# Kernel tuning notes

Measured on AMD Instinct MI355X. Metric: run time of the kernel, lower is better.

The kernel has to match this reference:

```python
import jax, jax.numpy as jnp
import numpy as np

N = 50000   # nodes
E = 1600000 # edges
G = 512     # graphs in batch
IN_DIM, EMBED, H, D = 64, 128, 4, 32
D1, D2, D3 = 128, 64, 16
NEG_SLOPE = 0.2  # DGL GATConv default


def setup_inputs() -> dict:
    key = jax.random.key(0)
    ks = jax.random.split(key, 16)
    def glorot(k, shape):
        fan = shape[0] + shape[-1]
        return jax.random.normal(k, shape, jnp.float32) * jnp.sqrt(2.0 / fan)
    return {
        "feature": jax.random.normal(ks[0], (N, IN_DIM), jnp.float32),
        "src": jax.random.randint(ks[1], (E,), 0, N, jnp.int32),
        "dst": jax.random.randint(ks[2], (E,), 0, N, jnp.int32),
        "graph_ids": jnp.sort(jax.random.randint(ks[3], (N,), 0, G, jnp.int32)),
        "W0": glorot(ks[4], (IN_DIM, EMBED)), "b0": jnp.zeros((EMBED,), jnp.float32),
        "Wfc": glorot(ks[5], (EMBED, H * D)),
        "attn_l": glorot(ks[6], (H, D)), "attn_r": glorot(ks[7], (H, D)),
        "gat_bias": jnp.zeros((H * D,), jnp.float32),
        "W1": glorot(ks[8], (H * D, D1)), "b1": jnp.zeros((D1,), jnp.float32),
        "W2": glorot(ks[9], (D1, D2)), "b2": jnp.zeros((D2,), jnp.float32),
        "W3": glorot(ks[10], (D2, D3)), "b3": jnp.zeros((D3,), jnp.float32),
    }


def reference(feature, src, dst, graph_ids, W0, b0, Wfc, attn_l, attn_r,
              gat_bias, W1, b1, W2, b2, W3, b3):
    # initial dense embed
    h = feature @ W0 + b0                                   # [N, EMBED]
    # GATConv
    feat = (h @ Wfc).reshape(N, H, D)                       # [N,H,D]
    el = jnp.einsum('nhd,hd->nh', feat, attn_l)             # [N,H]
    er = jnp.einsum('nhd,hd->nh', feat, attn_r)
    e = jax.nn.leaky_relu(el[src] + er[dst], NEG_SLOPE)     # [E,H]
    # segment softmax over incoming edges of each dst node
    m = jax.ops.segment_max(e, dst, num_segments=N)         # [N,H]
    ex = jnp.exp(e - m[dst])                                # [E,H]
    denom = jax.ops.segment_sum(ex, dst, num_segments=N)    # [N,H]
    a = ex / denom[dst]                                     # [E,H]
    msg = a[:, :, None] * feat[src]                         # [E,H,D]
    rst = jax.ops.segment_sum(msg, dst, num_segments=N)     # [N,H,D]
    rst = rst + gat_bias.reshape(1, H, D)
    hn = rst.reshape(N, H * D)
    # AvgPooling per graph
    sums = jax.ops.segment_sum(hn, graph_ids, num_segments=G)           # [G,H*D]
    cnts = jax.ops.segment_sum(jnp.ones((N,), hn.dtype), graph_ids, num_segments=G)
    hg = sums / jnp.maximum(cnts, 1.0)[:, None]
    # dense head
    out = jax.nn.elu(hg)
    out = jax.nn.elu(out @ W1 + b1)
    out = jax.nn.elu(out @ W2 + b2)
    out = out @ W3 + b3                                     # [G, D3]
    atten = a[:, :, None]                                   # [E,H,1] like DGL
    return out, atten
```

## Files before the change

kernel.cpp:

```cpp
#include <hip/hip_runtime.h>
#include <hip/hip_fp16.h>
#include <math.h>

#define N_NODES 50000
#define E_EDGES 1600000
#define G_GRAPHS 512
#define IN_DIM 64
#define EMBED 128
#define HD 128
#define NHEAD 4
#define D1 128
#define D2 64
#define D3 16
#define NEG_SLOPE 0.2f
#define NB ((N_NODES + 127) >> 7)
#define PT_TILE 4096
#define PT_BLOCKS ((E_EDGES + PT_TILE - 1) / PT_TILE)
#define FB_CAP 8192
#define M2_EDGE_BLK ((E_EDGES + 511) / 512)

typedef float vfloat4 __attribute__((ext_vector_type(4)));
typedef float vfloat2 __attribute__((ext_vector_type(2)));
typedef unsigned short ushort_t;

static __device__ __forceinline__ float leaky(float x) { return x > 0.f ? x : NEG_SLOPE * x; }

__global__ void __launch_bounds__(256) k0hg(const int* __restrict__ dst, int* __restrict__ ghist,
                                            const float* __restrict__ W0, const float* __restrict__ b0,
                                            const float* __restrict__ Wfc, float* __restrict__ Wc,
                                            float* __restrict__ bc) {
    __shared__ int lh[NB];
    const int t = threadIdx.x;
    if (blockIdx.x < PT_BLOCKS) {
        for (int i = t; i < NB; i += 256) lh[i] = 0;
        __syncthreads();
        const long e0 = (long)blockIdx.x * PT_TILE;
#pragma unroll
        for (int k = 0; k < PT_TILE / 256; ++k) {
            long e = e0 + t + k * 256;
            if (e < E_EDGES) atomicAdd(&lh[dst[e] >> 7], 1);
        }
        __syncthreads();
        for (int i = t; i < NB; i += 256) {
            int v = lh[i];
            if (v) atomicAdd(&ghist[i], v);
        }
    } else {
        int tid = (int)(blockIdx.x - PT_BLOCKS) * 256 + t;
        if (tid < IN_DIM * HD) {
            int i = tid >> 7, j = tid & 127;
            float acc = 0.f;
            for (int k = 0; k < EMBED; ++k) acc += W0[i * EMBED + k] * Wfc[k * HD + j];
            Wc[tid] = acc;
        } else if (tid < IN_DIM * HD + HD) {
            int j = tid - IN_DIM * HD;
            float acc = 0.f;
            for (int k = 0; k < EMBED; ++k) acc += b0[k] * Wfc[k * HD + j];
            bc[j] = acc;
        }
    }
}

__global__ void __launch_bounds__(256) k1_gemm(const float* __restrict__ A,
                                               const float* __restrict__ W,
                                               const float* __restrict__ b,
                                               const float* __restrict__ attn_l,
                                               const float* __restrict__ attn_r,
                                               unsigned char* __restrict__ feat,
                                               float* __restrict__ el,
                                               float* __restrict__ er) {
    __shared__ __align__(16) float Ws[IN_DIM * HD];
    __shared__ __align__(16) float As[64][68];
    const int t = threadIdx.x;
    const int cc = t & 31, rt = t >> 5;
    const int c0 = cc * 4, r0 = rt * 8;
    const int row0 = blockIdx.x * 64;

    {
        const float4* Wg = (const float4*)W;
        float4* Wl = (float4*)Ws;
#pragma unroll
        for (int j = 0; j < (IN_DIM * HD / 4) / 256; ++j) Wl[t + j * 256] = Wg[t + j * 256];
    }
#pragma unroll
    for (int j = 0; j < 4; ++j) {
        int i2 = t + j * 256;
        int row = i2 >> 4, kq = i2 & 15;
        int gr = row0 + row;
        float4 v = (gr < N_NODES) ? *(const float4*)(A + (size_t)gr * IN_DIM + kq * 4)
                                  : make_float4(0.f, 0.f, 0.f, 0.f);
        *(float4*)&As[row][kq * 4] = v;
    }
    __syncthreads();

    float acc[8][4];
#pragma unroll
    for (int i = 0; i < 8; ++i)
#pragma unroll
        for (int j = 0; j < 4; ++j) acc[i][j] = 0.f;

    for (int k4 = 0; k4 < IN_DIM / 4; ++k4) {
        vfloat4 w0 = *(const vfloat4*)&Ws[(k4 * 4 + 0) * HD + c0];
        vfloat4 w1 = *(const vfloat4*)&Ws[(k4 * 4 + 1) * HD + c0];
        vfloat4 w2 = *(const vfloat4*)&Ws[(k4 * 4 + 2) * HD + c0];
        vfloat4 w3 = *(const vfloat4*)&Ws[(k4 * 4 + 3) * HD + c0];
#pragma unroll
        for (int i = 0; i < 8; ++i) {
            vfloat4 a = *(const vfloat4*)&As[r0 + i][k4 * 4];
#pragma unroll
            for (int j = 0; j < 4; ++j)
                acc[i][j] += a.x * w0[j] + a.y * w1[j] + a.z * w2[j] + a.w * w3[j];
        }
    }
    {
        vfloat4 bcv = *(const vfloat4*)(b + c0);
#pragma unroll
        for (int i = 0; i < 8; ++i)
#pragma unroll
            for (int j = 0; j < 4; ++j) acc[i][j] += bcv[j];
    }
#pragma unroll
    for (int i = 0; i < 8; ++i) {
        int gr = row0 + r0 + i;
        if (gr < N_NODES) {
            unsigned int ww = __builtin_amdgcn_cvt_pk_fp8_f32(acc[i][0], acc[i][1], 0, false);
            ww = __builtin_amdgcn_cvt_pk_fp8_f32(acc[i][2], acc[i][3], ww, true);
            *(unsigned int*)(feat + (size_t)gr * HD + c0) = ww;
        }
    }
    {
        vfloat4 al = *(const vfloat4*)(attn_l + c0);
        vfloat4 ar = *(const vfloat4*)(attn_r + c0);
        float pl[8], pr[8];
#pragma unroll
        for (int i = 0; i < 8; ++i) {
            pl[i] = acc[i][0] * al[0] + acc[i][1] * al[1] + acc[i][2] * al[2] + acc[i][3] * al[3];
            pr[i] = acc[i][0] * ar[0] + acc[i][1] * ar[1] + acc[i][2] * ar[2] + acc[i][3] * ar[3];
        }
#pragma unroll
        for (int off = 1; off <= 4; off <<= 1) {
#pragma unroll
            for (int i = 0; i < 8; ++i) {
                pl[i] += __shfl_xor(pl[i], off);
                pr[i] += __shfl_xor(pr[i], off);
            }
        }
        if ((cc & 7) == 0) {
            const int h = cc >> 3;
#pragma unroll
            for (int i = 0; i < 8; ++i) {
                int gr = row0 + r0 + i;
                if (gr < N_NODES) {
                    el[gr * 4 + h] = pl[i];
                    er[gr * 4 + h] = pr[i];
                }
            }
        }
    }
}

__global__ void __launch_bounds__(256) pt_partition(const int* __restrict__ src,
                                                    const int* __restrict__ dst,
                                                    const int* __restrict__ ghist,
                                                    int* __restrict__ cursor0,
                                                    unsigned int* __restrict__ part) {
    __shared__ int hist[4][NB];
    __shared__ int tot[NB], offs[NB], base_s[NB];
    __shared__ int lcur[4][NB];
    __shared__ int gt[NB], offsG[NB];
    __shared__ unsigned int stage[PT_TILE];
    const int t = threadIdx.x, lane = t & 63, wid = t >> 6;
    const long e0 = (long)blockIdx.x * PT_TILE;
    const int cnt = (int)min((long)PT_TILE, (long)E_EDGES - e0);
    for (int i = t; i < NB; i += 256) {
        hist[0][i] = 0; hist[1][i] = 0; hist[2][i] = 0; hist[3][i] = 0;
        gt[i] = ghist[i];
    }
    __syncthreads();
    unsigned int v[PT_TILE / 256];
#pragma unroll
    for (int k = 0; k < PT_TILE / 256; ++k) {
        int i = t + k * 256;
        if (i < cnt) {
            int d = dst[e0 + i];
            v[k] = ((unsigned int)d << 16) | (unsigned int)src[e0 + i];
            atomicAdd(&hist[wid][d >> 7], 1);
        } else v[k] = 0xFFFFFFFFu;
    }
    __syncthreads();
    for (int i = t; i < NB; i += 256) {
        int h0 = hist[0][i], h1 = hist[1][i], h2 = hist[2][i], h3 = hist[3][i];
        hist[0][i] = 0; hist[1][i] = h0; hist[2][i] = h0 + h1; hist[3][i] = h0 + h1 + h2;
        tot[i] = h0 + h1 + h2 + h3;
    }
    __syncthreads();
    if (wid == 0) {
        int run = 0;
        for (int c = 0; c < (NB + 63) / 64; ++c) {
            int i = c * 64 + lane;
            int vv = (i < NB) ? tot[i] : 0;
            int incl = vv;
#pragma unroll
            for (int off = 1; off < 64; off <<= 1) {
                int o = __shfl_up(incl, off, 64);
                if (lane >= off) incl += o;
            }
            if (i < NB) offs[i] = run + incl - vv;
            run += __shfl(incl, 63, 64);
        }
    } else if (wid == 1) {
        int run = 0;
        for (int c = 0; c < (NB + 63) / 64; ++c) {
            int i = c * 64 + lane;
            int vv = (i < NB) ? gt[i] : 0;
            int incl = vv;
#pragma unroll
            for (int off = 1; off < 64; off <<= 1) {
                int o = __shfl_up(incl, off, 64);
                if (lane >= off) incl += o;
            }
            if (i < NB) offsG[i] = run + incl - vv;
            run += __shfl(incl, 63, 64);
        }
    }
    __syncthreads();
    for (int i = t; i < NB; i += 256) {
        int tt = tot[i];
        base_s[i] = offsG[i] + (tt ? atomicAdd(&cursor0[i], tt) : 0);
        int ob = offs[i];
        lcur[0][i] = ob + hist[0][i];
        lcur[1][i] = ob + hist[1][i];
        lcur[2][i] = ob + hist[2][i];
        lcur[3][i] = ob + hist[3][i];
    }
    __syncthreads();
#pragma unroll
    for (int k = 0; k < PT_TILE / 256; ++k) {
        if (v[k] != 0xFFFFFFFFu) {
            int b = v[k] >> 23;
            int pos = atomicAdd(&lcur[wid][b], 1);
            stage[pos] = v[k];
        }
    }
    __syncthreads();
    for (int i = t; i < cnt; i += 256) {
        unsigned int p = stage[i];
        int b = p >> 23;
        part[base_s[b] + (i - offs[b])] = p & 0x7FFFFFu;
    }
}

__global__ void __launch_bounds__(256) fb_fill(const unsigned int* __restrict__ part,
                                               const int* __restrict__ ghist,
                                               int* __restrict__ rowstart,
                                               ushort_t* __restrict__ csr_src) {
    const int b = blockIdx.x, t = threadIdx.x, lane = t & 63, wid = t >> 6;
    __shared__ int degl[4][128], totl[128], offl[128], curl[4][128];
    __shared__ int red[4], s0s[2];
    __shared__ ushort_t lsrc[FB_CAP];
    {
        int partial = 0;
        for (int i = t; i < b; i += 256) partial += ghist[i];
#pragma unroll
        for (int off = 32; off; off >>= 1) partial += __shfl_xor(partial, off);
        if (lane == 0) red[wid] = partial;
        if (t < 128) { degl[0][t] = 0; degl[1][t] = 0; degl[2][t] = 0; degl[3][t] = 0; }
        __syncthreads();
        if (t == 0) {
            int s0 = red[0] + red[1] + red[2] + red[3];
            s0s[0] = s0;
            s0s[1] = s0 + ghist[b];
        }
        __syncthreads();
    }
    const int s0 = s0s[0], s1 = s0s[1];
    const int cnt = s1 - s0;
    for (int i = t; i < cnt; i += 256) {
        unsigned int p = part[s0 + i];
        atomicAdd(&degl[wid][p >> 16], 1);
    }
    __syncthreads();
    if (t < 128) {
        int d0 = degl[0][t], d1 = degl[1][t], d2 = degl[2][t], d3 = degl[3][t];
        degl[0][t] = 0; degl[1][t] = d0; degl[2][t] = d0 + d1; degl[3][t] = d0 + d1 + d2;
        totl[t] = d0 + d1 + d2 + d3;
    }
    __syncthreads();
    if (wid == 0) {
        int run = 0;
        for (int c = 0; c < 2; ++c) {
            int i = c * 64 + lane;
            int vv = totl[i];
            int incl = vv;
#pragma unroll
            for (int off = 1; off < 64; off <<= 1) {
                int o = __shfl_up(incl, off, 64);
                if (lane >= off) incl += o;
            }
            offl[i] = run + incl - vv;
            run += __shfl(incl, 63, 64);
        }
    }
    __syncthreads();
    if (t < 128) {
        int ob = offl[t];
        curl[0][t] = ob + degl[0][t];
        curl[1][t] = ob + degl[1][t];
        curl[2][t] = ob + degl[2][t];
        curl[3][t] = ob + degl[3][t];
        int node = (b << 7) + t;
        if (node < N_NODES) rowstart[node] = s0 + ob;
    }
    if (b == 0 && t == 0) rowstart[N_NODES] = E_EDGES;
    __syncthreads();
    if (cnt <= FB_CAP) {
        for (int i = t; i < cnt; i += 256) {
            unsigned int p = part[s0 + i];
            int pos = atomicAdd(&curl[wid][p >> 16], 1);
            lsrc[pos] = (ushort_t)(p & 0xFFFFu);
        }
        __syncthreads();
        for (int i = t; i < cnt; i += 256) csr_src[s0 + i] = lsrc[i];
    } else {
        for (int i = t; i < cnt; i += 256) {
            unsigned int p = part[s0 + i];
            int pos = atomicAdd(&curl[wid][p >> 16], 1);
            csr_src[s0 + pos] = (ushort_t)(p & 0xFFFFu);
        }
    }
}

__global__ void __launch_bounds__(256) k6_aggregate(
    const ushort_t* __restrict__ csr_src, const int* __restrict__ rowstart,
    const float* __restrict__ el, const float* __restrict__ er,
    const unsigned char* __restrict__ feat, const float* __restrict__ gat_bias,
    float* __restrict__ er_rd, float* __restrict__ hn) {
    __shared__ uint2 s_pk[4][64][4];
    const int wid = threadIdx.x >> 6;
    const int lane = threadIdx.x & 63;
    const int n = blockIdx.x * 4 + wid;
    if (n >= N_NODES) return;
    const int start = rowstart[n];
    const int end = rowstart[n + 1];
    const int deg = end - start;

    const int e0 = lane >> 2;
    const int h = lane & 3;
    const float erh = er[n * 4 + h];
    float sm = 0.f;
    for (int base = 0; base < deg; base += 16) {
        const int e = base + e0;
        if (e < deg) {
            const int s = csr_src[start + e];
            const float ex = __expf(leaky(el[s * 4 + h] + erh));
            sm += ex;
            if (e < 64)
                s_pk[wid][e][h] = make_uint2((unsigned int)s << 7, __float_as_uint(ex));
        }
    }
#pragma unroll
    for (int off = 4; off <= 32; off <<= 1) sm += __shfl_xor(sm, off);
    const float rd = sm > 0.f ? 1.f / sm : 0.f;
    if (lane < 4) {
        er_rd[(size_t)n * 8 + lane] = erh;
        er_rd[(size_t)n * 8 + 4 + lane] = rd;
    }

    const int g4 = lane >> 4, gl = lane & 15;
    const int h2 = gl >> 2;
    const float rdh = __shfl(rd, h2);
    vfloat2 acc0 = {0.f, 0.f}, acc1 = {0.f, 0.f}, acc2 = {0.f, 0.f}, acc3 = {0.f, 0.f};

    if (deg <= 64) {
        const uint2* pk = &s_pk[wid][0][h2];
        const unsigned char* fg = feat + (gl << 3);
        int idx = g4;
        for (; idx + 4 < deg; idx += 8) {
            const uint2 pA = pk[idx * 4];
            const uint2 pB = pk[(idx + 4) * 4];
            const uint2 wA = *(const uint2*)(fg + pA.x);
            const uint2 wB = *(const uint2*)(fg + pB.x);
            const float exA = __uint_as_float(pA.y);
            const float exB = __uint_as_float(pB.y);
            const vfloat2 eA = {exA, exA}, eB = {exB, exB};
            acc0 += eA * __builtin_amdgcn_cvt_pk_f32_fp8(wA.x, false);
            acc1 += eA * __builtin_amdgcn_cvt_pk_f32_fp8(wA.x, true);
            acc2 += eA * __builtin_amdgcn_cvt_pk_f32_fp8(wA.y, false);
            acc3 += eA * __builtin_amdgcn_cvt_pk_f32_fp8(wA.y, true);
            acc0 += eB * __builtin_amdgcn_cvt_pk_f32_fp8(wB.x, false);
            acc1 += eB * __builtin_amdgcn_cvt_pk_f32_fp8(wB.x, true);
            acc2 += eB * __builtin_amdgcn_cvt_pk_f32_fp8(wB.y, false);
            acc3 += eB * __builtin_amdgcn_cvt_pk_f32_fp8(wB.y, true);
        }
        if (idx < deg) {
            const uint2 p = pk[idx * 4];
            const uint2 w = *(const uint2*)(fg + p.x);
            const float ex = __uint_as_float(p.y);
            const vfloat2 ev = {ex, ex};
            acc0 += ev * __builtin_amdgcn_cvt_pk_f32_fp8(w.x, false);
            acc1 += ev * __builtin_amdgcn_cvt_pk_f32_fp8(w.x, true);
            acc2 += ev * __builtin_amdgcn_cvt_pk_f32_fp8(w.y, false);
            acc3 += ev * __builtin_amdgcn_cvt_pk_f32_fp8(w.y, true);
        }
    } else {
        const float erh2 = __shfl(erh, h2);
        const unsigned char* fg = feat + (gl << 3);
        for (int e = start + g4; e < end; e += 4) {
            const unsigned int s = csr_src[e];
            const float ex = __expf(leaky(el[s * 4 + h2] + erh2));
            const vfloat2 ev = {ex, ex};
            const uint2 w = *(const uint2*)(fg + ((size_t)s << 7));
            acc0 += ev * __builtin_amdgcn_cvt_pk_f32_fp8(w.x, false);
            acc1 += ev * __builtin_amdgcn_cvt_pk_f32_fp8(w.x, true);
            acc2 += ev * __builtin_amdgcn_cvt_pk_f32_fp8(w.y, false);
            acc3 += ev * __builtin_amdgcn_cvt_pk_f32_fp8(w.y, true);
        }
    }
    {
        const vfloat2 rv = {rdh, rdh};
        acc0 *= rv; acc1 *= rv; acc2 *= rv; acc3 *= rv;
    }
#pragma unroll
    for (int off = 16; off <= 32; off <<= 1) {
        acc0.x += __shfl_xor(acc0.x, off);
        acc0.y += __shfl_xor(acc0.y, off);
        acc1.x += __shfl_xor(acc1.x, off);
        acc1.y += __shfl_xor(acc1.y, off);
        acc2.x += __shfl_xor(acc2.x, off);
        acc2.y += __shfl_xor(acc2.y, off);
        acc3.x += __shfl_xor(acc3.x, off);
        acc3.y += __shfl_xor(acc3.y, off);
    }
    if (lane < 16) {
        const float4 b0 = ((const float4*)gat_bias)[gl * 2];
        const float4 b1 = ((const float4*)gat_bias)[gl * 2 + 1];
        float4* hp = (float4*)(hn + (size_t)n * HD + gl * 8);
        hp[0] = make_float4(acc0.x + b0.x, acc0.y + b0.y, acc1.x + b0.z, acc1.y + b0.w);
        hp[1] = make_float4(acc2.x + b1.x, acc2.y + b1.y, acc3.x + b1.z, acc3.y + b1.w);
    }
}

__global__ void __launch_bounds__(512) m2b_mlp_attn(
    const int* __restrict__ src, const int* __restrict__ dst,
    const float* __restrict__ el, const float* __restrict__ er_rd,
    const float* __restrict__ hn, const int* __restrict__ graph_ids,
    const float* __restrict__ W1, const float* __restrict__ b1,
    const float* __restrict__ W2, const float* __restrict__ b2,
    const float* __restrict__ W3, const float* __restrict__ b3,
    float* __restrict__ a_out, float* __restrict__ out) {
    const int t = threadIdx.x;
    if (blockIdx.x < G_GRAPHS) {
        const int g = (int)blockIdx.x;
        const int tt = t & 127, part = t >> 7;
        __shared__ int bounds[2];
        __shared__ double pool[4][128];
        __shared__ double x[128], y[128];
        if (t < 2) {
            const int target = g + t;
            int lo = 0, hi = N_NODES;
            while (lo < hi) {
                int mid = (lo + hi) >> 1;
                if (graph_ids[mid] < target) lo = mid + 1; else hi = mid;
            }
            bounds[t] = lo;
        }
        __syncthreads();
        const int lo = bounds[0], hi = bounds[1];
        double s = 0.0;
        for (int n = lo + part; n < hi; n += 4) s += (double)hn[(size_t)n * HD + tt];
        pool[part][tt] = s;
        __syncthreads();
        if (t < 128) {
            const double cnt = (double)(hi - lo);
            const double sum = pool[0][t] + pool[1][t] + pool[2][t] + pool[3][t];
            const double v = sum / fmax(cnt, 1.0);
            x[t] = v > 0.0 ? v : expm1(v);
        }
        __syncthreads();
        if (t < 128) {
            double acc = (double)b1[t];
            for (int k = 0; k < HD; ++k) acc += x[k] * (double)W1[k * D1 + t];
            y[t] = acc > 0.0 ? acc : expm1(acc);
        }
        __syncthreads();
        if (t < D2) {
            double a2 = (double)b2[t];
            for (int k = 0; k < D1; ++k) a2 += y[k] * (double)W2[k * D2 + t];
            x[t] = a2 > 0.0 ? a2 : expm1(a2);
        }
        __syncthreads();
        if (t < D3) {
            double a3 = (double)b3[t];
            for (int k = 0; k < D2; ++k) a3 += x[k] * (double)W3[k * D3 + t];
            out[g * D3 + t] = (float)a3;
        }
    } else {
        const long e = (long)(blockIdx.x - G_GRAPHS) * 512 + t;
        if (e >= E_EDGES) return;
        const int s = src[e], d = dst[e];
        const float4 el4 = *(const float4*)(el + s * 4);
        const float4 er4 = *(const float4*)(er_rd + (size_t)d * 8);
        const float4 r4 = *(const float4*)(er_rd + (size_t)d * 8 + 4);
        vfloat4 a;
        a.x = __expf(leaky(el4.x + er4.x)) * r4.x;
        a.y = __expf(leaky(el4.y + er4.y)) * r4.y;
        a.z = __expf(leaky(el4.z + er4.z)) * r4.z;
        a.w = __expf(leaky(el4.w + er4.w)) * r4.w;
        __builtin_nontemporal_store(a, (vfloat4*)a_out + e);
    }
}

extern "C" void kernel_launch(void* const* d_in, const int* in_sizes, int n_in,
                              void* d_out, int out_size, void* d_ws, size_t ws_size,
                              hipStream_t stream) {
    const float* feature = (const float*)d_in[0];
    const int* src = (const int*)d_in[1];
    const int* dst = (const int*)d_in[2];
    const int* graph_ids = (const int*)d_in[3];
    const float* W0 = (const float*)d_in[4];
    const float* b0 = (const float*)d_in[5];
    const float* Wfc = (const float*)d_in[6];
    const float* attn_l = (const float*)d_in[7];
    const float* attn_r = (const float*)d_in[8];
    const float* gat_bias = (const float*)d_in[9];
    const float* W1 = (const float*)d_in[10];
    const float* b1 = (const float*)d_in[11];
    const float* W2 = (const float*)d_in[12];
    const float* b2 = (const float*)d_in[13];
    const float* W3 = (const float*)d_in[14];
    const float* b3 = (const float*)d_in[15];

    char* ws = (char*)d_ws;
    size_t off = 0;
    auto carve = [&](size_t bytes) -> void* {
        void* p = ws + off;
        off += (bytes + 255) & ~(size_t)255;
        return p;
    };
    int* ghist = (int*)carve((size_t)NB * 4);
    int* cursor0 = (int*)carve((size_t)NB * 4);
    const size_t zero_span = off;
    float* Wc = (float*)carve((size_t)IN_DIM * HD * 4);
    float* bc = (float*)carve((size_t)HD * 4);
    unsigned char* feat = (unsigned char*)carve((size_t)N_NODES * HD);
    float* el = (float*)carve((size_t)N_NODES * 4 * 4);
    float* er = (float*)carve((size_t)N_NODES * 4 * 4);
    float* er_rd = (float*)carve((size_t)N_NODES * 8 * 4);
    int* rowstart = (int*)carve((size_t)(N_NODES + 1) * 4);
    unsigned int* part = (unsigned int*)carve((size_t)E_EDGES * 4);
    ushort_t* csr_src = (ushort_t*)carve((size_t)E_EDGES * 2);
    float* hn = (float*)carve((size_t)N_NODES * HD * 4);

    float* out = (float*)d_out;
    float* a_out = out + G_GRAPHS * D3;

    (void)hipMemsetAsync(d_ws, 0, zero_span, stream);
    k0hg<<<PT_BLOCKS + 33, 256, 0, stream>>>(dst, ghist, W0, b0, Wfc, Wc, bc);
    k1_gemm<<<(N_NODES + 63) / 64, 256, 0, stream>>>(feature, Wc, bc, attn_l, attn_r,
                                                     feat, el, er);
    pt_partition<<<PT_BLOCKS, 256, 0, stream>>>(src, dst, ghist, cursor0, part);
    fb_fill<<<NB, 256, 0, stream>>>(part, ghist, rowstart, csr_src);
    k6_aggregate<<<(N_NODES + 3) / 4, 256, 0, stream>>>(csr_src, rowstart, el, er, feat,
                                                        gat_bias, er_rd, hn);
    m2b_mlp_attn<<<G_GRAPHS + M2_EDGE_BLK, 512, 0, stream>>>(src, dst, el, er_rd, hn,
                                                             graph_ids, W1, b1, W2, b2,
                                                             W3, b3, a_out, out);
}
```

Before: 234.3 us.

## Merge projection GEMM and edge partition into one launch; batch attention edges

The node-projection GEMM and the edge bucket-partition kernels now run as two block ranges of a single launch, sharing one shared-memory buffer carved per role. This removes a kernel boundary and lets the two independent stages overlap across CUs. The partition tile is doubled to 8192 edges per block, which means more work per block and a larger shared stage. The attention-output tail now handles four edges per thread, issuing all gathers before the math. The fused kernel's shared footprint is the maximum of both roles, so the GEMM blocks may lose occupancy.

```diff
diff --git a/kernel.cpp b/kernel.cpp
--- a/kernel.cpp
+++ b/kernel.cpp
@@ -14,10 +14,13 @@
 #define D3 16
 #define NEG_SLOPE 0.2f
 #define NB ((N_NODES + 127) >> 7)
-#define PT_TILE 4096
+#define HT_TILE 4096
+#define HT_BLOCKS ((E_EDGES + HT_TILE - 1) / HT_TILE)
+#define PT_TILE 8192
 #define PT_BLOCKS ((E_EDGES + PT_TILE - 1) / PT_TILE)
+#define K1_TILES ((N_NODES + 63) / 64)
 #define FB_CAP 8192
-#define M2_EDGE_BLK ((E_EDGES + 511) / 512)
+#define M2_EDGE_BLK ((E_EDGES + 2047) / 2048)
 
 typedef float vfloat4 __attribute__((ext_vector_type(4)));
 typedef float vfloat2 __attribute__((ext_vector_type(2)));
@@ -31,12 +34,12 @@
                                             float* __restrict__ bc) {
     __shared__ int lh[NB];
     const int t = threadIdx.x;
-    if (blockIdx.x < PT_BLOCKS) {
+    if (blockIdx.x < HT_BLOCKS) {
         for (int i = t; i < NB; i += 256) lh[i] = 0;
         __syncthreads();
-        const long e0 = (long)blockIdx.x * PT_TILE;
-#pragma unroll
-        for (int k = 0; k < PT_TILE / 256; ++k) {
+        const long e0 = (long)blockIdx.x * HT_TILE;
+#pragma unroll
+        for (int k = 0; k < HT_TILE / 256; ++k) {
             long e = e0 + t + k * 256;
             if (e < E_EDGES) atomicAdd(&lh[dst[e] >> 7], 1);
         }
@@ -46,7 +49,7 @@
             if (v) atomicAdd(&ghist[i], v);
         }
     } else {
-        int tid = (int)(blockIdx.x - PT_BLOCKS) * 256 + t;
+        int tid = (int)(blockIdx.x - HT_BLOCKS) * 256 + t;
         if (tid < IN_DIM * HD) {
             int i = tid >> 7, j = tid & 127;
             float acc = 0.f;
@@ -61,192 +64,191 @@
     }
 }
 
-__global__ void __launch_bounds__(256) k1_gemm(const float* __restrict__ A,
-                                               const float* __restrict__ W,
-                                               const float* __restrict__ b,
-                                               const float* __restrict__ attn_l,
-                                               const float* __restrict__ attn_r,
-                                               unsigned char* __restrict__ feat,
-                                               float* __restrict__ el,
-                                               float* __restrict__ er) {
-    __shared__ __align__(16) float Ws[IN_DIM * HD];
-    __shared__ __align__(16) float As[64][68];
+#define SMEM_BYTES 53248
+__global__ void __launch_bounds__(256) k1pt(
+    const float* __restrict__ A, const float* __restrict__ W,
+    const float* __restrict__ b, const float* __restrict__ attn_l,
+    const float* __restrict__ attn_r,
+    const int* __restrict__ src, const int* __restrict__ dst,
+    const int* __restrict__ ghist, int* __restrict__ cursor0,
+    unsigned char* __restrict__ feat, float* __restrict__ el,
+    float* __restrict__ er, unsigned int* __restrict__ part) {
+    __shared__ __align__(16) char smem[SMEM_BYTES];
     const int t = threadIdx.x;
-    const int cc = t & 31, rt = t >> 5;
-    const int c0 = cc * 4, r0 = rt * 8;
-    const int row0 = blockIdx.x * 64;
-
-    {
-        const float4* Wg = (const float4*)W;
-        float4* Wl = (float4*)Ws;
-#pragma unroll
-        for (int j = 0; j < (IN_DIM * HD / 4) / 256; ++j) Wl[t + j * 256] = Wg[t + j * 256];
-    }
-#pragma unroll
-    for (int j = 0; j < 4; ++j) {
-        int i2 = t + j * 256;
-        int row = i2 >> 4, kq = i2 & 15;
-        int gr = row0 + row;
-        float4 v = (gr < N_NODES) ? *(const float4*)(A + (size_t)gr * IN_DIM + kq * 4)
-                                  : make_float4(0.f, 0.f, 0.f, 0.f);
-        *(float4*)&As[row][kq * 4] = v;
-    }
-    __syncthreads();
-
-    float acc[8][4];
-#pragma unroll
-    for (int i = 0; i < 8; ++i)
-#pragma unroll
-        for (int j = 0; j < 4; ++j) acc[i][j] = 0.f;
-
-    for (int k4 = 0; k4 < IN_DIM / 4; ++k4) {
-        vfloat4 w0 = *(const vfloat4*)&Ws[(k4 * 4 + 0) * HD + c0];
-        vfloat4 w1 = *(const vfloat4*)&Ws[(k4 * 4 + 1) * HD + c0];
-        vfloat4 w2 = *(const vfloat4*)&Ws[(k4 * 4 + 2) * HD + c0];
-        vfloat4 w3 = *(const vfloat4*)&Ws[(k4 * 4 + 3) * HD + c0];
+    if (blockIdx.x < K1_TILES) {
+        float* Ws = (float*)smem;
+        float(*As)[68] = (float(*)[68])(smem + 32768);
+        const int cc = t & 31, rt = t >> 5;
+        const int c0 = cc * 4, r0 = rt * 8;
+        const int row0 = (int)blockIdx.x * 64;
+        {
+            const float4* Wg = (const float4*)W;
+            float4* Wl = (float4*)Ws;
+#pragma unroll
+            for (int j = 0; j < (IN_DIM * HD / 4) / 256; ++j) Wl[t + j * 256] = Wg[t + j * 256];
+        }
+#pragma unroll
+        for (int j = 0; j < 4; ++j) {
+            int i2 = t + j * 256;
+            int row = i2 >> 4, kq = i2 & 15;
+            int gr = row0 + row;
+            float4 v = (gr < N_NODES) ? *(const float4*)(A + (size_t)gr * IN_DIM + kq * 4)
+                                      : make_float4(0.f, 0.f, 0.f, 0.f);
+            *(float4*)&As[row][kq * 4] = v;
+        }
+        __syncthreads();
+        float acc[8][4];
+#pragma unroll
+        for (int i = 0; i < 8; ++i)
+#pragma unroll
+            for (int j = 0; j < 4; ++j) acc[i][j] = 0.f;
+        for (int k4 = 0; k4 < IN_DIM / 4; ++k4) {
+            vfloat4 w0 = *(const vfloat4*)&Ws[(k4 * 4 + 0) * HD + c0];
+            vfloat4 w1 = *(const vfloat4*)&Ws[(k4 * 4 + 1) * HD + c0];
+            vfloat4 w2 = *(const vfloat4*)&Ws[(k4 * 4 + 2) * HD + c0];
+            vfloat4 w3 = *(const vfloat4*)&Ws[(k4 * 4 + 3) * HD + c0];
+#pragma unroll
+            for (int i = 0; i < 8; ++i) {
+                vfloat4 a = *(const vfloat4*)&As[r0 + i][k4 * 4];
+#pragma unroll
+                for (int j = 0; j < 4; ++j)
+                    acc[i][j] += a.x * w0[j] + a.y * w1[j] + a.z * w2[j] + a.w * w3[j];
+            }
+        }
+        {
+            vfloat4 bcv = *(const vfloat4*)(b + c0);
+#pragma unroll
+            for (int i = 0; i < 8; ++i)
+#pragma unroll
+                for (int j = 0; j < 4; ++j) acc[i][j] += bcv[j];
+        }
 #pragma unroll
         for (int i = 0; i < 8; ++i) {
-            vfloat4 a = *(const vfloat4*)&As[r0 + i][k4 * 4];
-#pragma unroll
-            for (int j = 0; j < 4; ++j)
-                acc[i][j] += a.x * w0[j] + a.y * w1[j] + a.z * w2[j] + a.w * w3[j];
-        }
-    }
-    {
-        vfloat4 bcv = *(const vfloat4*)(b + c0);
-#pragma unroll
-        for (int i = 0; i < 8; ++i)
-#pragma unroll
-            for (int j = 0; j < 4; ++j) acc[i][j] += bcv[j];
-    }
-#pragma unroll
-    for (int i = 0; i < 8; ++i) {
-        int gr = row0 + r0 + i;
-        if (gr < N_NODES) {
-            unsigned int ww = __builtin_amdgcn_cvt_pk_fp8_f32(acc[i][0], acc[i][1], 0, false);
-            ww = __builtin_amdgcn_cvt_pk_fp8_f32(acc[i][2], acc[i][3], ww, true);
-            *(unsigned int*)(feat + (size_t)gr * HD + c0) = ww;
-        }
-    }
-    {
-        vfloat4 al = *(const vfloat4*)(attn_l + c0);
-        vfloat4 ar = *(const vfloat4*)(attn_r + c0);
-        float pl[8], pr[8];
-#pragma unroll
-        for (int i = 0; i < 8; ++i) {
-            pl[i] = acc[i][0] * al[0] + acc[i][1] * al[1] + acc[i][2] * al[2] + acc[i][3] * al[3];
-            pr[i] = acc[i][0] * ar[0] + acc[i][1] * ar[1] + acc[i][2] * ar[2] + acc[i][3] * ar[3];
-        }
-#pragma unroll
-        for (int off = 1; off <= 4; off <<= 1) {
+            int gr = row0 + r0 + i;
+            if (gr < N_NODES) {
+                unsigned int ww = __builtin_amdgcn_cvt_pk_fp8_f32(acc[i][0], acc[i][1], 0, false);
+                ww = __builtin_amdgcn_cvt_pk_fp8_f32(acc[i][2], acc[i][3], ww, true);
+                *(unsigned int*)(feat + (size_t)gr * HD + c0) = ww;
+            }
+        }
+        {
+            vfloat4 al = *(const vfloat4*)(attn_l + c0);
+            vfloat4 ar = *(const vfloat4*)(attn_r + c0);
+            float pl[8], pr[8];
 #pragma unroll
             for (int i = 0; i < 8; ++i) {
-                pl[i] += __shfl_xor(pl[i], off);
-                pr[i] += __shfl_xor(pr[i], off);
-            }
-        }
-        if ((cc & 7) == 0) {
-            const int h = cc >> 3;
-#pragma unroll
-            for (int i = 0; i < 8; ++i) {
-                int gr = row0 + r0 + i;
-                if (gr < N_NODES) {
-                    el[gr * 4 + h] = pl[i];
-                    er[gr * 4 + h] = pr[i];
+                pl[i] = acc[i][0] * al[0] + acc[i][1] * al[1] + acc[i][2] * al[2] + acc[i][3] * al[3];
+                pr[i] = acc[i][0] * ar[0] + acc[i][1] * ar[1] + acc[i][2] * ar[2] + acc[i][3] * ar[3];
+            }
+#pragma unroll
+            for (int off = 1; off <= 4; off <<= 1) {
+#pragma unroll
+                for (int i = 0; i < 8; ++i) {
+                    pl[i] += __shfl_xor(pl[i], off);
+                    pr[i] += __shfl_xor(pr[i], off);
                 }
             }
-        }
-    }
-}
-
-__global__ void __launch_bounds__(256) pt_partition(const int* __restrict__ src,
-                                                    const int* __restrict__ dst,
-                                                    const int* __restrict__ ghist,
-                                                    int* __restrict__ cursor0,
-                                                    unsigned int* __restrict__ part) {
-    __shared__ int hist[4][NB];
-    __shared__ int tot[NB], offs[NB], base_s[NB];
-    __shared__ int lcur[4][NB];
-    __shared__ int gt[NB], offsG[NB];
-    __shared__ unsigned int stage[PT_TILE];
-    const int t = threadIdx.x, lane = t & 63, wid = t >> 6;
-    const long e0 = (long)blockIdx.x * PT_TILE;
-    const int cnt = (int)min((long)PT_TILE, (long)E_EDGES - e0);
-    for (int i = t; i < NB; i += 256) {
-        hist[0][i] = 0; hist[1][i] = 0; hist[2][i] = 0; hist[3][i] = 0;
-        gt[i] = ghist[i];
-    }
-    __syncthreads();
-    unsigned int v[PT_TILE / 256];
-#pragma unroll
-    for (int k = 0; k < PT_TILE / 256; ++k) {
-        int i = t + k * 256;
-        if (i < cnt) {
-            int d = dst[e0 + i];
-            v[k] = ((unsigned int)d << 16) | (unsigned int)src[e0 + i];
-            atomicAdd(&hist[wid][d >> 7], 1);
-        } else v[k] = 0xFFFFFFFFu;
-    }
-    __syncthreads();
-    for (int i = t; i < NB; i += 256) {
-        int h0 = hist[0][i], h1 = hist[1][i], h2 = hist[2][i], h3 = hist[3][i];
-        hist[0][i] = 0; hist[1][i] = h0; hist[2][i] = h0 + h1; hist[3][i] = h0 + h1 + h2;
-        tot[i] = h0 + h1 + h2 + h3;
-    }
-    __syncthreads();
-    if (wid == 0) {
-        int run = 0;
-        for (int c = 0; c < (NB + 63) / 64; ++c) {
-            int i = c * 64 + lane;
-            int vv = (i < NB) ? tot[i] : 0;
-            int incl = vv;
-#pragma unroll
-            for (int off = 1; off < 64; off <<= 1) {
-                int o = __shfl_up(incl, off, 64);
-                if (lane >= off) incl += o;
-            }
-            if (i < NB) offs[i] = run + incl - vv;
-            run += __shfl(incl, 63, 64);
-        }
-    } else if (wid == 1) {
-        int run = 0;
-        for (int c = 0; c < (NB + 63) / 64; ++c) {
-            int i = c * 64 + lane;
-            int vv = (i < NB) ? gt[i] : 0;
-            int incl = vv;
-#pragma unroll
-            for (int off = 1; off < 64; off <<= 1) {
-                int o = __shfl_up(incl, off, 64);
-                if (lane >= off) incl += o;
-            }
-            if (i < NB) offsG[i] = run + incl - vv;
-            run += __shfl(incl, 63, 64);
-        }
-    }
-    __syncthreads();
-    for (int i = t; i < NB; i += 256) {
-        int tt = tot[i];
-        base_s[i] = offsG[i] + (tt ? atomicAdd(&cursor0[i], tt) : 0);
-        int ob = offs[i];
-        lcur[0][i] = ob + hist[0][i];
-        lcur[1][i] = ob + hist[1][i];
-        lcur[2][i] = ob + hist[2][i];
-        lcur[3][i] = ob + hist[3][i];
-    }
-    __syncthreads();
-#pragma unroll
-    for (int k = 0; k < PT_TILE / 256; ++k) {
-        if (v[k] != 0xFFFFFFFFu) {
-            int b = v[k] >> 23;
-            int pos = atomicAdd(&lcur[wid][b], 1);
-            stage[pos] = v[k];
-        }
-    }
-    __syncthreads();
-    for (int i = t; i < cnt; i += 256) {
-        unsigned int p = stage[i];
-        int b = p >> 23;
-        part[base_s[b] + (i - offs[b])] = p & 0x7FFFFFu;
+            if ((cc & 7) == 0) {
+                const int h = cc >> 3;
+#pragma unroll
+                for (int i = 0; i < 8; ++i) {
+                    int gr = row0 + r0 + i;
+                    if (gr < N_NODES) {
+                        el[gr * 4 + h] = pl[i];
+                        er[gr * 4 + h] = pr[i];
+                    }
+                }
+            }
+        }
+    } else {
+        int(*hist)[NB] = (int(*)[NB])smem;
+        int(*lcur)[NB] = (int(*)[NB])(smem + 6256);
+        int* tot = (int*)(smem + 12512);
+        int* offs = (int*)(smem + 14076);
+        int* base_s = (int*)(smem + 15640);
+        int* gt = (int*)(smem + 17204);
+        int* offsG = (int*)(smem + 18768);
+        unsigned int* stage = (unsigned int*)(smem + 20336);
+        const int lane = t & 63, wid = t >> 6;
+        const int tile = (int)blockIdx.x - K1_TILES;
+        const long e0 = (long)tile * PT_TILE;
+        const int cnt = (int)min((long)PT_TILE, (long)E_EDGES - e0);
+        for (int i = t; i < NB; i += 256) {
+            hist[0][i] = 0; hist[1][i] = 0; hist[2][i] = 0; hist[3][i] = 0;
+            gt[i] = ghist[i];
+        }
+        __syncthreads();
+        unsigned int v[PT_TILE / 256];
+#pragma unroll
+        for (int k = 0; k < PT_TILE / 256; ++k) {
+            int i = t + k * 256;
+            if (i < cnt) {
+                int d = dst[e0 + i];
+                v[k] = ((unsigned int)d << 16) | (unsigned int)src[e0 + i];
+                atomicAdd(&hist[wid][d >> 7], 1);
+            } else v[k] = 0xFFFFFFFFu;
+        }
+        __syncthreads();
+        for (int i = t; i < NB; i += 256) {
+            int h0 = hist[0][i], h1 = hist[1][i], h2 = hist[2][i], h3 = hist[3][i];
+            hist[0][i] = 0; hist[1][i] = h0; hist[2][i] = h0 + h1; hist[3][i] = h0 + h1 + h2;
+            tot[i] = h0 + h1 + h2 + h3;
+        }
+        __syncthreads();
+        if (wid == 0) {
+            int run = 0;
+            for (int c = 0; c < (NB + 63) / 64; ++c) {
+                int i = c * 64 + lane;
+                int vv = (i < NB) ? tot[i] : 0;
+                int incl = vv;
+#pragma unroll
+                for (int off = 1; off < 64; off <<= 1) {
+                    int o = __shfl_up(incl, off, 64);
+                    if (lane >= off) incl += o;
+                }
+                if (i < NB) offs[i] = run + incl - vv;
+                run += __shfl(incl, 63, 64);
+            }
+        } else if (wid == 1) {
+            int run = 0;
+            for (int c = 0; c < (NB + 63) / 64; ++c) {
+                int i = c * 64 + lane;
+                int vv = (i < NB) ? gt[i] : 0;
+                int incl = vv;
+#pragma unroll
+                for (int off = 1; off < 64; off <<= 1) {
+                    int o = __shfl_up(incl, off, 64);
+                    if (lane >= off) incl += o;
+                }
+                if (i < NB) offsG[i] = run + incl - vv;
+                run += __shfl(incl, 63, 64);
+            }
+        }
+        __syncthreads();
+        for (int i = t; i < NB; i += 256) {
+            int tt2 = tot[i];
+            base_s[i] = offsG[i] + (tt2 ? atomicAdd(&cursor0[i], tt2) : 0);
+            int ob = offs[i];
+            lcur[0][i] = ob + hist[0][i];
+            lcur[1][i] = ob + hist[1][i];
+            lcur[2][i] = ob + hist[2][i];
+            lcur[3][i] = ob + hist[3][i];
+        }
+        __syncthreads();
+#pragma unroll
+        for (int k = 0; k < PT_TILE / 256; ++k) {
+            if (v[k] != 0xFFFFFFFFu) {
+                int bb = v[k] >> 23;
+                int pos = atomicAdd(&lcur[wid][bb], 1);
+                stage[pos] = v[k];
+            }
+        }
+        __syncthreads();
+        for (int i = t; i < cnt; i += 256) {
+            unsigned int p = stage[i];
+            int bb = p >> 23;
+            part[base_s[bb] + (i - offs[bb])] = p & 0x7FFFFFu;
+        }
     }
 }
 
@@ -495,18 +497,35 @@
             out[g * D3 + t] = (float)a3;
         }
     } else {
-        const long e = (long)(blockIdx.x - G_GRAPHS) * 512 + t;
-        if (e >= E_EDGES) return;
-        const int s = src[e], d = dst[e];
-        const float4 el4 = *(const float4*)(el + s * 4);
-        const float4 er4 = *(const float4*)(er_rd + (size_t)d * 8);
-        const float4 r4 = *(const float4*)(er_rd + (size_t)d * 8 + 4);
-        vfloat4 a;
-        a.x = __expf(leaky(el4.x + er4.x)) * r4.x;
-        a.y = __expf(leaky(el4.y + er4.y)) * r4.y;
-        a.z = __expf(leaky(el4.z + er4.z)) * r4.z;
-        a.w = __expf(leaky(el4.w + er4.w)) * r4.w;
-        __builtin_nontemporal_store(a, (vfloat4*)a_out + e);
+        const long base = (long)(blockIdx.x - G_GRAPHS) * 2048 + t;
+        bool ok[4];
+        int sx[4], dx[4];
+#pragma unroll
+        for (int k = 0; k < 4; ++k) {
+            const long e = base + (long)k * 512;
+            ok[k] = e < E_EDGES;
+            const long ei = ok[k] ? e : 0;
+            sx[k] = src[ei];
+            dx[k] = dst[ei];
+        }
+        float4 el4[4], er4[4], r4[4];
+#pragma unroll
+        for (int k = 0; k < 4; ++k) {
+            el4[k] = *(const float4*)(el + sx[k] * 4);
+            er4[k] = *(const float4*)(er_rd + (size_t)dx[k] * 8);
+            r4[k] = *(const float4*)(er_rd + (size_t)dx[k] * 8 + 4);
+        }
+#pragma unroll
+        for (int k = 0; k < 4; ++k) {
+            if (ok[k]) {
+                vfloat4 a;
+                a.x = __expf(leaky(el4[k].x + er4[k].x)) * r4[k].x;
+                a.y = __expf(leaky(el4[k].y + er4[k].y)) * r4[k].y;
+                a.z = __expf(leaky(el4[k].z + er4[k].z)) * r4[k].z;
+                a.w = __expf(leaky(el4[k].w + er4[k].w)) * r4[k].w;
+                __builtin_nontemporal_store(a, (vfloat4*)a_out + (base + (long)k * 512));
+            }
+        }
     }
 }
 
@@ -555,10 +574,10 @@
     float* a_out = out + G_GRAPHS * D3;
 
     (void)hipMemsetAsync(d_ws, 0, zero_span, stream);
-    k0hg<<<PT_BLOCKS + 33, 256, 0, stream>>>(dst, ghist, W0, b0, Wfc, Wc, bc);
-    k1_gemm<<<(N_NODES + 63) / 64, 256, 0, stream>>>(feature, Wc, bc, attn_l, attn_r,
-                                                     feat, el, er);
-    pt_partition<<<PT_BLOCKS, 256, 0, stream>>>(src, dst, ghist, cursor0, part);
+    k0hg<<<HT_BLOCKS + 33, 256, 0, stream>>>(dst, ghist, W0, b0, Wfc, Wc, bc);
+    k1pt<<<K1_TILES + PT_BLOCKS, 256, 0, stream>>>(feature, Wc, bc, attn_l, attn_r,
+                                                   src, dst, ghist, cursor0,
+                                                   feat, el, er, part);
     fb_fill<<<NB, 256, 0, stream>>>(part, ghist, rowstart, csr_src);
     k6_aggregate<<<(N_NODES + 3) / 4, 256, 0, stream>>>(csr_src, rowstart, el, er, feat,
                                                         gat_bias, er_rd, hn);
```

After: 227.6 us. 2.8% less time.
